# Optimization experiments

Measured on AMD Instinct MI355X. Metric: run time of the kernel, lower is better.

## Reference

```python
import jax, jax.numpy as jnp
import numpy as np

B, A, F, D, C = 256, 128, 512, 6, 512  # batch, max_atoms, atom_features, max_degree, conv_width


def setup_inputs() -> dict:
    key = jax.random.key(0)
    k1, k2, k3, k4 = jax.random.split(key, 4)
    atoms = jax.random.normal(k1, (B, A, F), dtype=jnp.float32)
    # neighbour indices in [0, A); pad entries beyond each atom's degree with -1
    neigh = jax.random.randint(k2, (B, A, D), 0, A)
    deg = jax.random.randint(k3, (B, A, 1), 0, D)  # degrees in 0..D-1
    bonds = jnp.where(jnp.arange(D)[None, None, :] < deg, neigh, -1)
    # one Dense(conv_width) per degree: stacked kernels [D, F, C] and biases [D, C]
    W = jax.random.normal(k4, (D, F, C), dtype=jnp.float32) * 0.02
    b = jnp.zeros((D, C), dtype=jnp.float32)
    return {"atoms": atoms, "bonds": bonds, "W": W, "b": b}


def reference(atoms, bonds, W, b):
    d_max = bonds.shape[-1]
    # per-atom degree = count of non -1 neighbour slots  [B, A, 1]
    degrees = jnp.sum(bonds != -1, axis=-1, keepdims=True)
    # shift lookup by 1 so that padded (-1) neighbours index a zero row
    padded = jnp.pad(atoms, ((0, 0), (1, 1), (0, 0)))  # [B, A+2, F]
    idx = bonds + 1  # [B, A, D]
    # per-sample gather of neighbour features -> [B, A, D, F]
    neigh_feats = jax.vmap(lambda ref, i: ref[i])(padded, idx)
    summed = jnp.sum(neigh_feats, axis=2) + atoms  # [B, A, F]
    # apply all degree-specific dense layers, then mask-select by degree
    dense = jnp.einsum('baf,dfc->badc', summed, W) + b  # [B, A, D, C]
    masks = (degrees[..., None] == jnp.arange(d_max).reshape(1, 1, d_max, 1)).astype(dense.dtype)
    return jnp.sum(dense * masks, axis=2)  # [B, A, C]
```

## Files before the change

kernel.cpp:

```cpp
#include <hip/hip_runtime.h>
#include <hip/hip_bf16.h>


#define NB 256
#define NA 128
#define NF 512
#define ND 6
#define NC 512
#define NATOMS (NB * NA)

#define NT_TRANS 1536
#define NT_BUCK  32
#define NT_SUM   8192

typedef __attribute__((ext_vector_type(8))) short frag8;
typedef __attribute__((ext_vector_type(4))) float f32x4;

static __device__ inline unsigned short f2bu(float f) {
    __hip_bfloat16 h = __float2bfloat16(f);
    return *reinterpret_cast<unsigned short*>(&h);
}
static __device__ inline unsigned int pack2(float a, float b) {
    return (unsigned int)f2bu(a) | ((unsigned int)f2bu(b) << 16);
}
static __device__ inline void async16(const void* g, void* l) {
    __builtin_amdgcn_global_load_lds(
        (const __attribute__((address_space(1))) void*)g,
        (__attribute__((address_space(3))) void*)l, 16, 0, 0);
}

__global__ __launch_bounds__(256) void prep(
    const float* __restrict__ W, __hip_bfloat16* __restrict__ Wt,
    const int* __restrict__ bonds, int* __restrict__ counts,
    int* __restrict__ bucket,
    const float* __restrict__ atoms, __hip_bfloat16* __restrict__ summed) {
    const int bid = blockIdx.x;
    const int tid = threadIdx.x;
    __shared__ float t[32][33];
    __shared__ int lcnt[ND];
    __shared__ int lbase[ND];

    if (bid < NT_TRANS) {
        const int tx = tid & 31, ty = tid >> 5;
        const int c0 = (bid & 15) * 32;
        const int f0 = ((bid >> 4) & 15) * 32;
        const int d  = bid >> 8;
        #pragma unroll
        for (int r = 0; r < 32; r += 8)
            t[ty + r][tx] =
                W[((size_t)(d * NF + f0 + ty + r)) * NC + c0 + tx];
        __syncthreads();
        #pragma unroll
        for (int r = 0; r < 32; r += 8)
            Wt[((size_t)(d * NC + c0 + ty + r)) * NF + f0 + tx] =
                __float2bfloat16(t[tx][ty + r]);
        return;
    }
    if (bid < NT_TRANS + NT_BUCK) {
        const int b = bid - NT_TRANS;
        if (tid < ND) lcnt[tid] = 0;
        __syncthreads();
        int deg[4], loc[4], gg[4];
        #pragma unroll
        for (int i = 0; i < 4; ++i) {
            int g = b * 1024 + i * 256 + tid;
            gg[i] = g;
            int dg = 0;
            #pragma unroll
            for (int j = 0; j < ND; ++j) dg += (bonds[g * ND + j] >= 0);
            deg[i] = dg;
            loc[i] = atomicAdd(&lcnt[dg], 1);
        }
        __syncthreads();
        if (tid < ND) lbase[tid] = atomicAdd(&counts[tid], lcnt[tid]);
        __syncthreads();
        #pragma unroll
        for (int i = 0; i < 4; ++i)
            bucket[deg[i] * NATOMS + lbase[deg[i]] + loc[i]] = gg[i];
        return;
    }
    const int sbid = bid - (NT_TRANS + NT_BUCK);
    const int wave = tid >> 6;
    const int lane = tid & 63;
    const int swz  = (sbid & 7) * (NT_SUM / 8) + (sbid >> 3);
    const int g    = swz * 4 + wave;
    const float4* a4 = (const float4*)atoms;

    int   nb[ND];
    float msk[ND];
    #pragma unroll
    for (int j = 0; j < ND; ++j) {
        int n = bonds[g * ND + j];
        msk[j] = (n >= 0) ? 1.0f : 0.0f;
        nb[j]  = (n >= 0) ? n : 0;
    }
    const int rowbase = g & ~(NA - 1);

    float4 s0 = a4[(size_t)g * 128 + lane];
    float4 s1 = a4[(size_t)g * 128 + 64 + lane];
    float4 v0[ND], v1[ND];
    #pragma unroll
    for (int j = 0; j < ND; ++j) {
        const size_t base = (size_t)(rowbase + nb[j]) * 128;
        v0[j] = a4[base + lane];
        v1[j] = a4[base + 64 + lane];
    }
    #pragma unroll
    for (int j = 0; j < ND; ++j) {
        s0.x = fmaf(v0[j].x, msk[j], s0.x); s0.y = fmaf(v0[j].y, msk[j], s0.y);
        s0.z = fmaf(v0[j].z, msk[j], s0.z); s0.w = fmaf(v0[j].w, msk[j], s0.w);
        s1.x = fmaf(v1[j].x, msk[j], s1.x); s1.y = fmaf(v1[j].y, msk[j], s1.y);
        s1.z = fmaf(v1[j].z, msk[j], s1.z); s1.w = fmaf(v1[j].w, msk[j], s1.w);
    }

    uint2 o0, o1;
    o0.x = pack2(s0.x, s0.y); o0.y = pack2(s0.z, s0.w);
    o1.x = pack2(s1.x, s1.y); o1.y = pack2(s1.z, s1.w);
    ((uint2*)summed)[(size_t)g * 128 + lane] = o0;
    ((uint2*)summed)[(size_t)g * 128 + 64 + lane] = o1;
}

__global__ __launch_bounds__(256, 3) void gemm_deg(
    const __hip_bfloat16* __restrict__ summed, const __hip_bfloat16* __restrict__ Wt,
    const float* __restrict__ bias, const int* __restrict__ counts,
    const int* __restrict__ bucket, float* __restrict__ out) {
    const int L  = blockIdx.x + 24 * blockIdx.y;
    const int q  = L >> 3;
    const int p  = ((q >> 2) << 3) + (L & 7);
    const int d  = p % ND;
    const int m0 = (p / ND) * 128;
    const int n0 = (q & 3) * 128;
    const int Md = counts[d];
    if (m0 >= Md) return;

    __shared__ __align__(16) __hip_bfloat16 sA[3][128 * 32];
    __shared__ __align__(16) __hip_bfloat16 sB[3][128 * 32];
    __shared__ int sRows[128];

    const int tid = threadIdx.x;
    if (tid < 128) {
        int r = m0 + tid;
        sRows[tid] = (r < Md) ? bucket[d * NATOMS + r] : -1;
    }
    __syncthreads();

    const int lane = tid & 63;
    const int w    = tid >> 6;

    const int srow2 = tid >> 2;
    const int slot  = tid & 3;
    const int gs    = slot ^ ((srow2 >> 1) & 3);

    const char* smB = (const char*)summed;
    const char* wtB = (const char*)Wt + (size_t)(d * NC + n0) * (NF * 2);
    size_t gA[2];
    #pragma unroll
    for (int c = 0; c < 2; ++c) {
        int qr = sRows[c * 64 + srow2];
        gA[c] = (size_t)((qr < 0) ? 0 : qr) * (NF * 2);
    }

    const int quad = lane >> 4, l16 = lane & 15;
    const int xr2  = (l16 >> 1) & 3;
    const int wy = w >> 1, wx = w & 1;

    f32x4 acc[4][4];
    #pragma unroll
    for (int i = 0; i < 4; ++i)
        #pragma unroll
        for (int j = 0; j < 4; ++j) acc[i][j] = (f32x4)0.0f;

    auto stage = [&](int buf, int kt) {
        const int koff = kt * 64 + gs * 16;
        #pragma unroll
        for (int c = 0; c < 2; ++c) {
            async16(smB + gA[c] + koff, &sA[buf][c * 2048 + w * 512]);
            async16(wtB + (size_t)(c * 64 + srow2) * (NF * 2) + koff,
                    &sB[buf][c * 2048 + w * 512]);
        }
    };
    auto compute = [&](int buf) {
        frag8 aF[4], bF[4];
        #pragma unroll
        for (int i = 0; i < 4; ++i)
            aF[i] = *(const frag8*)&sA[buf][(wy * 64 + i * 16 + l16) * 32 +
                                            ((quad ^ xr2) << 3)];
        #pragma unroll
        for (int j = 0; j < 4; ++j)
            bF[j] = *(const frag8*)&sB[buf][(wx * 64 + j * 16 + l16) * 32 +
                                            ((quad ^ xr2) << 3)];
        #pragma unroll
        for (int i = 0; i < 4; ++i)
            #pragma unroll
            for (int j = 0; j < 4; ++j)
                acc[i][j] = __builtin_amdgcn_mfma_f32_16x16x32_bf16(
                    aF[i], bF[j], acc[i][j], 0, 0, 0);
    };

    stage(0, 0);
    stage(1, 1);
    #pragma unroll
    for (int kt = 0; kt < NF / 32; ++kt) {
        if (kt < NF / 32 - 1)
            asm volatile("s_waitcnt vmcnt(4)" ::: "memory");
        else
            asm volatile("s_waitcnt vmcnt(0)" ::: "memory");
        __builtin_amdgcn_sched_barrier(0);
        __builtin_amdgcn_s_barrier();
        if (kt + 2 < NF / 32) stage((kt + 2) % 3, kt + 2);
        __builtin_amdgcn_s_setprio(1);
        compute(kt % 3);
        __builtin_amdgcn_s_setprio(0);
    }

    #pragma unroll
    for (int j = 0; j < 4; ++j) {
        const int n = n0 + wx * 64 + j * 16 + l16;
        const float bv = bias[d * NC + n];
        #pragma unroll
        for (int i = 0; i < 4; ++i) {
            #pragma unroll
            for (int r = 0; r < 4; ++r) {
                const int tr = wy * 64 + i * 16 + quad * 4 + r;
                const int g  = sRows[tr];
                if (g >= 0)
                    out[(size_t)g * NC + n] = acc[i][j][r] + bv;
            }
        }
    }
}

extern "C" void kernel_launch(void* const* d_in, const int* in_sizes, int n_in,
                              void* d_out, int out_size, void* d_ws, size_t ws_size,
                              hipStream_t stream) {
    const float* atoms = (const float*)d_in[0];
    const int*   bonds = (const int*)d_in[1];
    const float* W     = (const float*)d_in[2];
    const float* bias  = (const float*)d_in[3];
    float* out = (float*)d_out;

    char* ws = (char*)d_ws;
    int* counts = (int*)ws;
    int* bucket = (int*)(ws + 1024);
    __hip_bfloat16* Wt     = (__hip_bfloat16*)(ws + 1024 + 786432);
    __hip_bfloat16* summed = (__hip_bfloat16*)(ws + 1024 + 786432 + 3145728);

    hipMemsetAsync(counts, 0, 1024, stream);

    prep<<<NT_TRANS + NT_BUCK + NT_SUM, 256, 0, stream>>>(
        W, Wt, bonds, counts, bucket, atoms, summed);

    gemm_deg<<<dim3(24, NATOMS / 128), 256, 0, stream>>>(
        summed, Wt, bias, counts, bucket, out);
}
```

Before: 176.8 us.

## Load MFMA fragments directly from global memory, dropping LDS staging

Removes the LDS triple-buffered async global-to-LDS staging in the degree-bucketed GEMM. Each wave now loads its A and B bf16 fragments straight from global memory into registers, using a two-deep register double buffer. This drops the block barriers and LDS traffic, but each wave fetches its fragments on its own, so data the block used to share is reloaded, raising global/L2 traffic and register pressure.

```diff
diff --git a/kernel.cpp b/kernel.cpp
--- a/kernel.cpp
+++ b/kernel.cpp
@@ -22,11 +22,6 @@
 }
 static __device__ inline unsigned int pack2(float a, float b) {
     return (unsigned int)f2bu(a) | ((unsigned int)f2bu(b) << 16);
-}
-static __device__ inline void async16(const void* g, void* l) {
-    __builtin_amdgcn_global_load_lds(
-        (const __attribute__((address_space(1))) void*)g,
-        (__attribute__((address_space(3))) void*)l, 16, 0, 0);
 }
 
 __global__ __launch_bounds__(256) void prep(
@@ -133,10 +128,7 @@
     const int Md = counts[d];
     if (m0 >= Md) return;
 
-    __shared__ __align__(16) __hip_bfloat16 sA[3][128 * 32];
-    __shared__ __align__(16) __hip_bfloat16 sB[3][128 * 32];
     __shared__ int sRows[128];
-
     const int tid = threadIdx.x;
     if (tid < 128) {
         int r = m0 + tid;
@@ -146,23 +138,21 @@
 
     const int lane = tid & 63;
     const int w    = tid >> 6;
-
-    const int srow2 = tid >> 2;
-    const int slot  = tid & 3;
-    const int gs    = slot ^ ((srow2 >> 1) & 3);
+    const int quad = lane >> 4, l16 = lane & 15;
+    const int wy = w >> 1, wx = w & 1;
 
     const char* smB = (const char*)summed;
     const char* wtB = (const char*)Wt + (size_t)(d * NC + n0) * (NF * 2);
-    size_t gA[2];
-    #pragma unroll
-    for (int c = 0; c < 2; ++c) {
-        int qr = sRows[c * 64 + srow2];
-        gA[c] = (size_t)((qr < 0) ? 0 : qr) * (NF * 2);
-    }
-
-    const int quad = lane >> 4, l16 = lane & 15;
-    const int xr2  = (l16 >> 1) & 3;
-    const int wy = w >> 1, wx = w & 1;
+    const char* pA[4];
+    const char* pB[4];
+    #pragma unroll
+    for (int i = 0; i < 4; ++i) {
+        int g = sRows[wy * 64 + i * 16 + l16];
+        pA[i] = smB + (size_t)((g < 0) ? 0 : g) * 1024 + quad * 16;
+    }
+    #pragma unroll
+    for (int j = 0; j < 4; ++j)
+        pB[j] = wtB + (size_t)(wx * 64 + j * 16 + l16) * 1024 + quad * 16;
 
     f32x4 acc[4][4];
     #pragma unroll
@@ -170,46 +160,30 @@
         #pragma unroll
         for (int j = 0; j < 4; ++j) acc[i][j] = (f32x4)0.0f;
 
-    auto stage = [&](int buf, int kt) {
-        const int koff = kt * 64 + gs * 16;
-        #pragma unroll
-        for (int c = 0; c < 2; ++c) {
-            async16(smB + gA[c] + koff, &sA[buf][c * 2048 + w * 512]);
-            async16(wtB + (size_t)(c * 64 + srow2) * (NF * 2) + koff,
-                    &sB[buf][c * 2048 + w * 512]);
+    frag8 aP[2][4], bP[2][4];
+    #pragma unroll
+    for (int i = 0; i < 4; ++i) aP[0][i] = *(const frag8*)(pA[i]);
+    #pragma unroll
+    for (int j = 0; j < 4; ++j) bP[0][j] = *(const frag8*)(pB[j]);
+
+    #pragma unroll
+    for (int kt = 0; kt < NF / 32; ++kt) {
+        const int cur = kt & 1, nxt = cur ^ 1;
+        if (kt + 1 < NF / 32) {
+            #pragma unroll
+            for (int i = 0; i < 4; ++i)
+                aP[nxt][i] = *(const frag8*)(pA[i] + (kt + 1) * 64);
+            #pragma unroll
+            for (int j = 0; j < 4; ++j)
+                bP[nxt][j] = *(const frag8*)(pB[j] + (kt + 1) * 64);
         }
-    };
-    auto compute = [&](int buf) {
-        frag8 aF[4], bF[4];
-        #pragma unroll
-        for (int i = 0; i < 4; ++i)
-            aF[i] = *(const frag8*)&sA[buf][(wy * 64 + i * 16 + l16) * 32 +
-                                            ((quad ^ xr2) << 3)];
-        #pragma unroll
-        for (int j = 0; j < 4; ++j)
-            bF[j] = *(const frag8*)&sB[buf][(wx * 64 + j * 16 + l16) * 32 +
-                                            ((quad ^ xr2) << 3)];
+        __builtin_amdgcn_s_setprio(1);
         #pragma unroll
         for (int i = 0; i < 4; ++i)
             #pragma unroll
             for (int j = 0; j < 4; ++j)
                 acc[i][j] = __builtin_amdgcn_mfma_f32_16x16x32_bf16(
-                    aF[i], bF[j], acc[i][j], 0, 0, 0);
-    };
-
-    stage(0, 0);
-    stage(1, 1);
-    #pragma unroll
-    for (int kt = 0; kt < NF / 32; ++kt) {
-        if (kt < NF / 32 - 1)
-            asm volatile("s_waitcnt vmcnt(4)" ::: "memory");
-        else
-            asm volatile("s_waitcnt vmcnt(0)" ::: "memory");
-        __builtin_amdgcn_sched_barrier(0);
-        __builtin_amdgcn_s_barrier();
-        if (kt + 2 < NF / 32) stage((kt + 2) % 3, kt + 2);
-        __builtin_amdgcn_s_setprio(1);
-        compute(kt % 3);
+                    aP[cur][i], bP[cur][j], acc[i][j], 0, 0, 0);
         __builtin_amdgcn_s_setprio(0);
     }
 
```

After: 217.3 us. 1.23x slower.

## Stage molecules in LDS for neighbour sum and enlarge GEMM M-tile to 256

Applied to the files above, without the earlier changes.

The neighbour summation moves out of the prep kernel into a new per-molecule kernel. It loads all 128 atoms of a molecule into swizzled LDS as bf16, then gathers the neighbours from LDS instead of re-reading fp32 rows from global memory for every neighbour. This cuts the sevenfold global and L2 traffic, but atoms are now rounded to bf16 before summing, and the kernel adds a launch and uses 128KB of LDS per block. The degree-bucketed GEMM now runs 512 threads with 256x128 tiles, so each weight tile is reused across twice as many rows. The load schedule and waitcnt are adjusted to match.

```diff
diff --git a/kernel.cpp b/kernel.cpp
--- a/kernel.cpp
+++ b/kernel.cpp
@@ -11,7 +11,6 @@
 
 #define NT_TRANS 1536
 #define NT_BUCK  32
-#define NT_SUM   8192
 
 typedef __attribute__((ext_vector_type(8))) short frag8;
 typedef __attribute__((ext_vector_type(4))) float f32x4;
@@ -22,6 +21,11 @@
 }
 static __device__ inline unsigned int pack2(float a, float b) {
     return (unsigned int)f2bu(a) | ((unsigned int)f2bu(b) << 16);
+}
+static __device__ inline float b2f(unsigned short u) {
+    __hip_bfloat16 h;
+    *reinterpret_cast<unsigned short*>(&h) = u;
+    return __bfloat162float(h);
 }
 static __device__ inline void async16(const void* g, void* l) {
     __builtin_amdgcn_global_load_lds(
@@ -29,11 +33,10 @@
         (__attribute__((address_space(3))) void*)l, 16, 0, 0);
 }
 
-__global__ __launch_bounds__(256) void prep(
+__global__ __launch_bounds__(256) void prep_misc(
     const float* __restrict__ W, __hip_bfloat16* __restrict__ Wt,
     const int* __restrict__ bonds, int* __restrict__ counts,
-    int* __restrict__ bucket,
-    const float* __restrict__ atoms, __hip_bfloat16* __restrict__ summed) {
+    int* __restrict__ bucket) {
     const int bid = blockIdx.x;
     const int tid = threadIdx.x;
     __shared__ float t[32][33];
@@ -56,71 +59,84 @@
                 __float2bfloat16(t[tx][ty + r]);
         return;
     }
-    if (bid < NT_TRANS + NT_BUCK) {
-        const int b = bid - NT_TRANS;
-        if (tid < ND) lcnt[tid] = 0;
-        __syncthreads();
-        int deg[4], loc[4], gg[4];
-        #pragma unroll
-        for (int i = 0; i < 4; ++i) {
-            int g = b * 1024 + i * 256 + tid;
-            gg[i] = g;
-            int dg = 0;
-            #pragma unroll
-            for (int j = 0; j < ND; ++j) dg += (bonds[g * ND + j] >= 0);
-            deg[i] = dg;
-            loc[i] = atomicAdd(&lcnt[dg], 1);
-        }
-        __syncthreads();
-        if (tid < ND) lbase[tid] = atomicAdd(&counts[tid], lcnt[tid]);
-        __syncthreads();
-        #pragma unroll
-        for (int i = 0; i < 4; ++i)
-            bucket[deg[i] * NATOMS + lbase[deg[i]] + loc[i]] = gg[i];
-        return;
-    }
-    const int sbid = bid - (NT_TRANS + NT_BUCK);
-    const int wave = tid >> 6;
-    const int lane = tid & 63;
-    const int swz  = (sbid & 7) * (NT_SUM / 8) + (sbid >> 3);
-    const int g    = swz * 4 + wave;
-    const float4* a4 = (const float4*)atoms;
-
-    int   nb[ND];
+    const int b = bid - NT_TRANS;
+    if (tid < ND) lcnt[tid] = 0;
+    __syncthreads();
+    int deg[4], loc[4], gg[4];
+    #pragma unroll
+    for (int i = 0; i < 4; ++i) {
+        int g = b * 1024 + i * 256 + tid;
+        gg[i] = g;
+        int dg = 0;
+        #pragma unroll
+        for (int j = 0; j < ND; ++j) dg += (bonds[g * ND + j] >= 0);
+        deg[i] = dg;
+        loc[i] = atomicAdd(&lcnt[dg], 1);
+    }
+    __syncthreads();
+    if (tid < ND) lbase[tid] = atomicAdd(&counts[tid], lcnt[tid]);
+    __syncthreads();
+    #pragma unroll
+    for (int i = 0; i < 4; ++i)
+        bucket[deg[i] * NATOMS + lbase[deg[i]] + loc[i]] = gg[i];
+}
+
+__global__ __launch_bounds__(512, 2) void sum_mol(
+    const float* __restrict__ atoms, const int* __restrict__ bonds,
+    __hip_bfloat16* __restrict__ summed) {
+    __shared__ __align__(16) __hip_bfloat16 mol[NA * NF];
+    char* molB = (char*)mol;
+    const int m   = blockIdx.x;
+    const int tid = threadIdx.x;
+
+    const float4* a4 = (const float4*)atoms + (size_t)m * (NA * NF / 4);
+    #pragma unroll 4
+    for (int i = 0; i < 32; ++i) {
+        float4 v = a4[i * 512 + tid];
+        const int r  = i * 4 + (tid >> 7);
+        const int co = tid & 127;
+        uint2 pk; pk.x = pack2(v.x, v.y); pk.y = pack2(v.z, v.w);
+        *(uint2*)(molB + r * 1024 + (((co >> 1) ^ (r & 7)) << 4) + (co & 1) * 8) = pk;
+    }
+    __syncthreads();
+
+    const int a  = tid >> 2;
+    const int qd = tid & 3;
+    const int* bd = bonds + (size_t)(m * NA + a) * ND;
+    int   nb[ND], x7[ND];
     float msk[ND];
     #pragma unroll
     for (int j = 0; j < ND; ++j) {
-        int n = bonds[g * ND + j];
+        int n = bd[j];
         msk[j] = (n >= 0) ? 1.0f : 0.0f;
         nb[j]  = (n >= 0) ? n : 0;
-    }
-    const int rowbase = g & ~(NA - 1);
-
-    float4 s0 = a4[(size_t)g * 128 + lane];
-    float4 s1 = a4[(size_t)g * 128 + 64 + lane];
-    float4 v0[ND], v1[ND];
-    #pragma unroll
-    for (int j = 0; j < ND; ++j) {
-        const size_t base = (size_t)(rowbase + nb[j]) * 128;
-        v0[j] = a4[base + lane];
-        v1[j] = a4[base + 64 + lane];
-    }
-    #pragma unroll
-    for (int j = 0; j < ND; ++j) {
-        s0.x = fmaf(v0[j].x, msk[j], s0.x); s0.y = fmaf(v0[j].y, msk[j], s0.y);
-        s0.z = fmaf(v0[j].z, msk[j], s0.z); s0.w = fmaf(v0[j].w, msk[j], s0.w);
-        s1.x = fmaf(v1[j].x, msk[j], s1.x); s1.y = fmaf(v1[j].y, msk[j], s1.y);
-        s1.z = fmaf(v1[j].z, msk[j], s1.z); s1.w = fmaf(v1[j].w, msk[j], s1.w);
-    }
-
-    uint2 o0, o1;
-    o0.x = pack2(s0.x, s0.y); o0.y = pack2(s0.z, s0.w);
-    o1.x = pack2(s1.x, s1.y); o1.y = pack2(s1.z, s1.w);
-    ((uint2*)summed)[(size_t)g * 128 + lane] = o0;
-    ((uint2*)summed)[(size_t)g * 128 + 64 + lane] = o1;
-}
-
-__global__ __launch_bounds__(256, 3) void gemm_deg(
+        x7[j]  = nb[j] & 7;
+    }
+    const int a7 = a & 7;
+    char* outB = (char*)summed + (size_t)(m * NA + a) * 1024;
+
+    #pragma unroll 4
+    for (int ci = 0; ci < 16; ++ci) {
+        const int c = qd * 16 + ci;
+        const frag8 s = *(const frag8*)(molB + a * 1024 + ((c ^ a7) << 4));
+        float acc[8];
+        #pragma unroll
+        for (int e = 0; e < 8; ++e) acc[e] = b2f((unsigned short)s[e]);
+        #pragma unroll
+        for (int j = 0; j < ND; ++j) {
+            const frag8 v = *(const frag8*)(molB + nb[j] * 1024 + ((c ^ x7[j]) << 4));
+            #pragma unroll
+            for (int e = 0; e < 8; ++e)
+                acc[e] = fmaf(b2f((unsigned short)v[e]), msk[j], acc[e]);
+        }
+        uint4 o;
+        o.x = pack2(acc[0], acc[1]); o.y = pack2(acc[2], acc[3]);
+        o.z = pack2(acc[4], acc[5]); o.w = pack2(acc[6], acc[7]);
+        *(uint4*)(outB + c * 16) = o;
+    }
+}
+
+__global__ __launch_bounds__(512, 4) void gemm_deg(
     const __hip_bfloat16* __restrict__ summed, const __hip_bfloat16* __restrict__ Wt,
     const float* __restrict__ bias, const int* __restrict__ counts,
     const int* __restrict__ bucket, float* __restrict__ out) {
@@ -128,17 +144,17 @@
     const int q  = L >> 3;
     const int p  = ((q >> 2) << 3) + (L & 7);
     const int d  = p % ND;
-    const int m0 = (p / ND) * 128;
+    const int m0 = (p / ND) * 256;
     const int n0 = (q & 3) * 128;
     const int Md = counts[d];
     if (m0 >= Md) return;
 
-    __shared__ __align__(16) __hip_bfloat16 sA[3][128 * 32];
+    __shared__ __align__(16) __hip_bfloat16 sA[3][256 * 32];
     __shared__ __align__(16) __hip_bfloat16 sB[3][128 * 32];
-    __shared__ int sRows[128];
+    __shared__ int sRows[256];
 
     const int tid = threadIdx.x;
-    if (tid < 128) {
+    if (tid < 256) {
         int r = m0 + tid;
         sRows[tid] = (r < Md) ? bucket[d * NATOMS + r] : -1;
     }
@@ -147,18 +163,19 @@
     const int lane = tid & 63;
     const int w    = tid >> 6;
 
-    const int srow2 = tid >> 2;
-    const int slot  = tid & 3;
-    const int gs    = slot ^ ((srow2 >> 1) & 3);
-
+    const int sr = lane >> 2;
+    const int sl = lane & 3;
+    const int gseg = sl ^ ((sr >> 1) & 3);
+
+    const int rA0 = w * 16 + sr;
+    const int rA1 = 128 + rA0;
+    const int rB  = w * 16 + sr;
     const char* smB = (const char*)summed;
-    const char* wtB = (const char*)Wt + (size_t)(d * NC + n0) * (NF * 2);
-    size_t gA[2];
-    #pragma unroll
-    for (int c = 0; c < 2; ++c) {
-        int qr = sRows[c * 64 + srow2];
-        gA[c] = (size_t)((qr < 0) ? 0 : qr) * (NF * 2);
-    }
+    const char* wtB = (const char*)Wt + (size_t)(d * NC + n0) * 1024;
+    int g0 = sRows[rA0], g1 = sRows[rA1];
+    const size_t gA0 = (size_t)((g0 < 0) ? 0 : g0) * 1024;
+    const size_t gA1 = (size_t)((g1 < 0) ? 0 : g1) * 1024;
+    const size_t gB  = (size_t)rB * 1024;
 
     const int quad = lane >> 4, l16 = lane & 15;
     const int xr2  = (l16 >> 1) & 3;
@@ -171,13 +188,10 @@
         for (int j = 0; j < 4; ++j) acc[i][j] = (f32x4)0.0f;
 
     auto stage = [&](int buf, int kt) {
-        const int koff = kt * 64 + gs * 16;
-        #pragma unroll
-        for (int c = 0; c < 2; ++c) {
-            async16(smB + gA[c] + koff, &sA[buf][c * 2048 + w * 512]);
-            async16(wtB + (size_t)(c * 64 + srow2) * (NF * 2) + koff,
-                    &sB[buf][c * 2048 + w * 512]);
-        }
+        const int koff = kt * 64 + gseg * 16;
+        async16(smB + gA0 + koff, (char*)&sA[buf][0] + w * 1024);
+        async16(smB + gA1 + koff, (char*)&sA[buf][0] + 8192 + w * 1024);
+        async16(wtB + gB  + koff, (char*)&sB[buf][0] + w * 1024);
     };
     auto compute = [&](int buf) {
         frag8 aF[4], bF[4];
@@ -202,7 +216,7 @@
     #pragma unroll
     for (int kt = 0; kt < NF / 32; ++kt) {
         if (kt < NF / 32 - 1)
-            asm volatile("s_waitcnt vmcnt(4)" ::: "memory");
+            asm volatile("s_waitcnt vmcnt(3)" ::: "memory");
         else
             asm volatile("s_waitcnt vmcnt(0)" ::: "memory");
         __builtin_amdgcn_sched_barrier(0);
@@ -247,9 +261,10 @@
 
     hipMemsetAsync(counts, 0, 1024, stream);
 
-    prep<<<NT_TRANS + NT_BUCK + NT_SUM, 256, 0, stream>>>(
-        W, Wt, bonds, counts, bucket, atoms, summed);
-
-    gemm_deg<<<dim3(24, NATOMS / 128), 256, 0, stream>>>(
+    prep_misc<<<NT_TRANS + NT_BUCK, 256, 0, stream>>>(W, Wt, bonds, counts, bucket);
+
+    sum_mol<<<NB, 512, 0, stream>>>(atoms, bonds, summed);
+
+    gemm_deg<<<dim3(24, 128), 512, 0, stream>>>(
         summed, Wt, bias, counts, bucket, out);
 }
```

Result: no change. 174.7 us (-1.2%).
